# Optimization experiments

Measured on AMD Instinct MI355X. Metric: run time of the kernel, lower is better.

## Reference

```python
import jax, jax.numpy as jnp
import numpy as np

B, T, D = 4, 4096, 384
H = W = 64
K = 8            # num_clusters
CH = MH = 64     # conv_hidden, mlp_hidden
NL = 4           # num_layers
IN_DIM = D + 2   # use_spatial_pos
RADIUS_FRACTION = 30.0
GRAPH_EPS = 1e-6
SM_LAMBDA = 0.01
FS_LAMBDA = 0.09


def conv2d(x, w, b, groups=1):
    out = jax.lax.conv_general_dilated(x, w, (1, 1), 'SAME',
        dimension_numbers=('NCHW', 'OIHW', 'NCHW'), feature_group_count=groups)
    return out + b[None, :, None, None]


def group_norm(x, g, b, groups, eps=1e-5):
    n, c, h, w = x.shape
    xg = x.reshape(n, groups, c // groups, h, w)
    m = xg.mean(axis=(2, 3, 4), keepdims=True)
    v = xg.var(axis=(2, 3, 4), keepdims=True)
    xn = ((xg - m) * jax.lax.rsqrt(v + eps)).reshape(n, c, h, w)
    return xn * g[None, :, None, None] + b[None, :, None, None]


def layer_norm(x, g, b, eps=1e-5):
    m = x.mean(-1, keepdims=True)
    v = x.var(-1, keepdims=True)
    return (x - m) * jax.lax.rsqrt(v + eps) * g + b


def build_graph():
    # unit-square grid positions; radius graph with self loops; sym normalization
    lin = jnp.linspace(0.0, 1.0, H)
    gy, gx = jnp.meshgrid(lin, lin, indexing='ij')
    pos = jnp.stack([gx.reshape(-1), gy.reshape(-1)], axis=1)  # (T,2)
    r2 = 2.0 / (RADIUS_FRACTION * RADIUS_FRACTION)             # (sqrt(2)/rf)^2
    dx = pos[:, 0][:, None] - pos[:, 0][None, :]
    dy = pos[:, 1][:, None] - pos[:, 1][None, :]
    adj = ((dx * dx + dy * dy) <= r2).astype(jnp.float32)      # includes loop
    deg = adj.sum(1)
    dis = jnp.where(deg > 0, deg ** -0.5, 0.0)
    a_tilde = dis[:, None] * adj * dis[None, :]                # D^-1/2 A D^-1/2
    return pos, a_tilde


def setup_inputs():
    key = jax.random.key(0)
    ks = jax.random.split(key, 16)
    rn = lambda i, s, sc=0.05: jax.random.normal(ks[i], s, dtype=jnp.float32) * sc
    z = lambda s: jnp.zeros(s, jnp.float32)
    o = lambda s: jnp.ones(s, jnp.float32)
    return {
        'token_features': jax.random.normal(ks[0], (B, T, D), dtype=jnp.float32),
        'gcn_w0': rn(1, (IN_DIM, CH)), 'gcn_b0': z((CH,)),
        'gcn_w': rn(2, (NL - 1, CH, CH)), 'gcn_b': z((NL - 1, CH)),
        'ln_g': o((NL, CH)), 'ln_b': z((NL, CH)),
        'res_w': rn(3, (IN_DIM, CH)), 'res_b': z((CH,)),
        'res_ln_g': o((CH,)), 'res_ln_b': z((CH,)),
        'mlp_w1': rn(4, (CH, MH)), 'mlp_b1': z((MH,)),
        'mlp_ln_g': o((MH,)), 'mlp_ln_b': z((MH,)),
        'mlp_w2': rn(5, (MH, K)), 'mlp_b2': z((K,)),
        'sm_w1': rn(6, (K, 1, 3, 3)), 'sm_b1': z((K,)),
        'sm_gn1_g': o((K,)), 'sm_gn1_b': z((K,)),
        'sm_w2': rn(7, (K, 1, 3, 3)), 'sm_b2': z((K,)),
        'sm_gn2_g': o((K,)), 'sm_gn2_b': z((K,)),
        'ec_w1': rn(8, (32, D, 3, 3), 0.02), 'ec_b1': z((32,)),
        'ec_gn_g': o((32,)), 'ec_gn_b': z((32,)),
        'ec_w2': rn(9, (1, 32, 1, 1)), 'ec_b2': z((1,)),
        'k': 8,
    }


def reference(token_features, gcn_w0, gcn_b0, gcn_w, gcn_b, ln_g, ln_b,
              res_w, res_b, res_ln_g, res_ln_b, mlp_w1, mlp_b1, mlp_ln_g,
              mlp_ln_b, mlp_w2, mlp_b2, sm_w1, sm_b1, sm_gn1_g, sm_gn1_b,
              sm_w2, sm_b2, sm_gn2_g, sm_gn2_b, ec_w1, ec_b1, ec_gn_g,
              ec_gn_b, ec_w2, ec_b2, k):
    pos, A = build_graph()

    # ---- feature smoothness loss (edge-aware) ----
    fs = token_features.reshape(B, H, W, D).transpose(0, 3, 1, 2)  # (B,D,H,W)
    e = jax.nn.relu(group_norm(conv2d(fs, ec_w1, ec_b1), ec_gn_g, ec_gn_b, 8))
    ew = jax.nn.sigmoid(conv2d(e, ec_w2, ec_b2))                   # (B,1,H,W)
    gy = fs[:, :, 1:, :] - fs[:, :, :-1, :]
    gx = fs[:, :, :, 1:] - fs[:, :, :, :-1]
    loss_y = (gy * gy * ew[:, :, 1:, :]).mean() / D
    loss_x = (gx * gx * ew[:, :, :, 1:]).mean() / D
    feat_sm = (loss_y + loss_x) / 2

    # ---- GNN pool (batched; adjacency shared across batch) ----
    x = jnp.concatenate(
        [token_features, jnp.broadcast_to(pos[None], (B, T, 2))], axis=-1)
    Ws = [gcn_w0] + [gcn_w[i] for i in range(NL - 1)]
    bs = [gcn_b0] + [gcn_b[i] for i in range(NL - 1)]
    for i in range(NL):
        x_prev = x
        h = jnp.einsum('ts,bsc->btc', A, x @ Ws[i]) + bs[i]  # GCNConv
        h = jax.nn.elu(layer_norm(h, ln_g[i], ln_b[i]))
        if i == 0:
            x_prev = layer_norm(x_prev @ res_w + res_b, res_ln_g, res_ln_b)
        x = h + x_prev
    h1 = jax.nn.elu(layer_norm(x @ mlp_w1 + mlp_b1, mlp_ln_g, mlp_ln_b))
    S = jax.nn.softmax(h1 @ mlp_w2 + mlp_b2, axis=-1)        # (B,T,K)

    # ---- spatial smoothness loss (depthwise convs) ----
    S_sp = S.transpose(0, 2, 1).reshape(B, K, H, W)
    t = jax.nn.relu(group_norm(conv2d(S_sp, sm_w1, sm_b1, groups=K),
                               sm_gn1_g, sm_gn1_b, K))
    S_sm = group_norm(conv2d(t, sm_w2, sm_b2, groups=K), sm_gn2_g, sm_gn2_b, K)
    sm_loss = ((S_sm - S_sp) ** 2).mean(axis=(1, 2, 3))      # (B,)

    # ---- normalized-cut + orthogonality losses ----
    AS = jnp.einsum('ts,bsk->btk', A, S)
    num = jnp.einsum('btk,btk->b', S, AS)
    degA = A.sum(1)
    den = jnp.einsum('btk,t,btk->b', S, degA, S) + GRAPH_EPS
    loss_c = -num / den
    SS = jnp.einsum('btk,btl->bkl', S, S)
    ssn = jnp.sqrt((SS * SS).sum(axis=(1, 2)))
    eyeK = jnp.eye(K, dtype=jnp.float32)
    target = eyeK / (jnp.sqrt(jnp.float32(K)) + GRAPH_EPS)
    diff = SS / (ssn[:, None, None] + GRAPH_EPS) - target[None]
    loss_o = jnp.sqrt((diff * diff).sum(axis=(1, 2)))

    loss = (loss_c + loss_o + SM_LAMBDA * sm_loss).mean() + FS_LAMBDA * feat_sm
    return S, loss
```

## Files before the change

### kernel.cpp

```cpp
#include <hip/hip_runtime.h>
#include <hip/hip_bf16.h>


#define B_ 4
#define T_ 4096
#define D_ 384

typedef __attribute__((ext_vector_type(8))) short short8b;
typedef __attribute__((ext_vector_type(4))) float f32x4;

__device__ __forceinline__ float wred(float v) {
#pragma unroll
  for (int off = 32; off > 0; off >>= 1) v += __shfl_xor(v, off);
  return v;
}

__device__ __forceinline__ void wred2(float& a, float& b) {
#pragma unroll
  for (int off = 32; off > 0; off >>= 1) {
    a += __shfl_xor(a, off);
    b += __shfl_xor(b, off);
  }
}

__device__ __forceinline__ short bf16rne(float f) {
  unsigned u = __float_as_uint(f);
  unsigned r = (u + 0x7FFFu + ((u >> 16) & 1u)) >> 16;
  return (short)r;
}

__device__ __forceinline__ float bf2f(short s) {
  return __uint_as_float(((unsigned)(unsigned short)s) << 16);
}

__device__ __forceinline__ float uval(int i) {
  int c = (i < 2 ? i : 2) + ((63 - i) < 2 ? (63 - i) : 2) + 1;
  return rsqrtf((float)c);
}

struct PGcn {
  const float *feat, *ecw1, *w0, *resw, *resb, *resg, *reslb;
  const float *gw, *gb0, *gb, *lng, *lnb;
  const float *w1, *b1, *mlng, *mlnb, *w2, *b2;
  short *fb, *wq, *wb;
  float *accg, *xwA, *xwB, *xbuf, *resbuf, *S, *Sp;
};

struct PLoss {
  const float *S, *Sp;
  const float *smw1, *smb1, *smg1, *smbb1, *smw2, *smb2, *smg2, *smbb2;
  const short *fb, *wq;
  const float *ecb1;
  float *eraw, *accg;
  const float *gng, *gnb, *ecw2, *ecb2;
  float *ew, *outp;
};


__device__ __forceinline__ void prep_stage(int blk, int tid,
    const float* feat, const float* ecw1, const float* w0, const float* resw,
    short* fb, short* wq, short* wb, float* accg) {
  if (blk == 0) {
    accg[tid] = 0.f;
    accg[tid + 256] = 0.f;
  }
  if (blk < 3072) {
    int t = blk * 256 + tid;
    const float4* s = (const float4*)feat + (size_t)t * 2;
    float4 a = s[0], b = s[1];
    short8b v;
    v[0] = bf16rne(a.x); v[1] = bf16rne(a.y); v[2] = bf16rne(a.z); v[3] = bf16rne(a.w);
    v[4] = bf16rne(b.x); v[5] = bf16rne(b.y); v[6] = bf16rne(b.z); v[7] = bf16rne(b.w);
    *(short8b*)(fb + (size_t)t * 8) = v;
  } else if (blk < 3504) {
    int idx = (blk - 3072) * 256 + tid;
    int q = idx % 9;
    int rest = idx / 9;
    int d = rest % 384;
    int o = rest / 384;
    wq[((size_t)(q * 32 + o)) * 384 + d] = bf16rne(ecw1[idx]);
  } else {
    int u = (blk - 3504) * 256 + tid;
    int l = u & 63, f = (u >> 6) & 7, s = u >> 9;
    int c = f * 16 + (l & 15);
    int k0 = s * 32 + ((l >> 4) << 3);
    const float* src = (c < 64) ? (w0 + c) : (resw + (c - 64));
    short8b v;
#pragma unroll
    for (int j = 0; j < 8; ++j) v[j] = bf16rne(src[(size_t)(k0 + j) * 64]);
    *(short8b*)(wb + (size_t)u * 8) = v;
  }
}

__device__ __forceinline__ void gemm0_stage(char* smem, int blk, int tid,
    const short* fb, const short* wb, const float* w0, const float* resw,
    const float* resb, const float* resg, const float* reslb,
    float* xw, float* res) {
  short8b* Ab8 = (short8b*)smem;
  short8b* Bb8 = (short8b*)(smem + 24576);
  int row0 = blk * 32;
#pragma unroll
  for (int it = 0; it < 6; ++it) {
    int u = it * 256 + tid;
    int l = u & 63, s = (u >> 6) % 12, set = u / 768;
    int row = row0 + set * 16 + (l & 15);
    int k = s * 32 + ((l >> 4) << 3);
    Ab8[(set * 12 + s) * 64 + l] = *(const short8b*)(fb + (size_t)row * 384 + k);
  }
  int wid = tid >> 6, lane = tid & 63;
  int rowset = wid & 1, colhalf = wid >> 1;
  const short8b* wb8 = (const short8b*)wb;
  f32x4 acc[4];
#pragma unroll
  for (int f = 0; f < 4; ++f) acc[f] = (f32x4){0.f, 0.f, 0.f, 0.f};
  for (int c = 0; c < 3; ++c) {
    __syncthreads();
#pragma unroll
    for (int it = 0; it < 8; ++it) {
      int u = it * 256 + tid;
      Bb8[u] = wb8[c * 2048 + u];
    }
    __syncthreads();
#pragma unroll
    for (int s = 0; s < 4; ++s) {
      short8b av = Ab8[(rowset * 12 + c * 4 + s) * 64 + lane];
#pragma unroll
      for (int f = 0; f < 4; ++f) {
        short8b bv = Bb8[(s * 8 + colhalf * 4 + f) * 64 + lane];
        acc[f] = __builtin_amdgcn_mfma_f32_16x16x32_bf16(av, bv, acc[f], 0, 0, 0);
      }
    }
  }
  int g = lane >> 4, ln = lane & 15;
  if (colhalf == 0) {
    float pw1[4], pw2[4];
#pragma unroll
    for (int f = 0; f < 4; ++f) {
      int c = f * 16 + ln;
      pw1[f] = w0[384 * 64 + c];
      pw2[f] = w0[385 * 64 + c];
    }
#pragma unroll
    for (int r = 0; r < 4; ++r) {
      int grow = row0 + rowset * 16 + g * 4 + r;
      int t = grow & (T_ - 1);
      float px = (float)(t & 63) * (1.f / 63.f);
      float py = (float)(t >> 6) * (1.f / 63.f);
#pragma unroll
      for (int f = 0; f < 4; ++f)
        xw[(size_t)grow * 64 + f * 16 + ln] = acc[f][r] + px * pw1[f] + py * pw2[f];
    }
  } else {
    float rw1[4], rw2[4], rb[4], rgam[4], rbet[4];
#pragma unroll
    for (int f = 0; f < 4; ++f) {
      int c = f * 16 + ln;
      rw1[f] = resw[384 * 64 + c];
      rw2[f] = resw[385 * 64 + c];
      rb[f] = resb[c]; rgam[f] = resg[c]; rbet[f] = reslb[c];
    }
#pragma unroll
    for (int r = 0; r < 4; ++r) {
      int grow = row0 + rowset * 16 + g * 4 + r;
      int t = grow & (T_ - 1);
      float px = (float)(t & 63) * (1.f / 63.f);
      float py = (float)(t >> 6) * (1.f / 63.f);
      float rv[4];
      float s1 = 0.f, s2 = 0.f;
#pragma unroll
      for (int f = 0; f < 4; ++f) {
        float v = acc[f][r] + px * rw1[f] + py * rw2[f] + rb[f];
        rv[f] = v;
        s1 += v;
        s2 = fmaf(v, v, s2);
      }
#pragma unroll
      for (int off = 1; off < 16; off <<= 1) {
        s1 += __shfl_xor(s1, off);
        s2 += __shfl_xor(s2, off);
      }
      float mean = s1 * (1.f / 64.f);
      float var = s2 * (1.f / 64.f) - mean * mean;
      float inv = rsqrtf(var + 1e-5f);
#pragma unroll
      for (int f = 0; f < 4; ++f)
        res[(size_t)grow * 64 + f * 16 + ln] =
            (rv[f] - mean) * inv * rgam[f] + rbet[f];
    }
  }
}

__device__ __forceinline__ void layer_stage(char* smem, int blk, int tid,
    const float* xw_in, const float* W, const float* bias, const float* lng,
    const float* lnb, const float* resid, float* xout, float* xw_out) {
  float* sx = (float*)smem;
  float* sW = (float*)(smem + 8192);
  int t0 = blk * 32;
  int b = t0 >> 12, i = (t0 >> 6) & 63;
  const float4* w4 = (const float4*)W;
  float4* sW4 = (float4*)sW;
#pragma unroll
  for (int l = 0; l < 4; ++l) sW4[tid + l * 256] = w4[tid + l * 256];
  int c = tid & 63, jg = tid >> 6;
  int jb = (t0 & 63) + jg * 8;
  float ui = uval(i);
  float acc[8];
#pragma unroll
  for (int m = 0; m < 8; ++m) acc[m] = 0.f;
  float uw[12];
#pragma unroll
  for (int d = 0; d < 12; ++d) {
    int jj = jb - 2 + d;
    uw[d] = (jj >= 0 && jj < 64) ? uval(jj) : 0.f;
  }
#pragma unroll
  for (int di = -2; di <= 2; ++di) {
    int ii = i + di;
    if (ii < 0 || ii > 63) continue;
    float wi = uval(ii);
    const float* src = xw_in + ((size_t)((b << 12) + (ii << 6))) * 64 + c;
    float v[12];
#pragma unroll
    for (int d = 0; d < 12; ++d) {
      int jj = jb - 2 + d;
      v[d] = (jj >= 0 && jj < 64) ? src[jj * 64] : 0.f;
    }
#pragma unroll
    for (int m = 0; m < 8; ++m) {
      float t = v[m] * uw[m] + v[m + 1] * uw[m + 1] + v[m + 2] * uw[m + 2] +
                v[m + 3] * uw[m + 3] + v[m + 4] * uw[m + 4];
      acc[m] = fmaf(wi, t, acc[m]);
    }
  }
  float bc = bias[c], gam = lng[c], bet = lnb[c];
#pragma unroll
  for (int m = 0; m < 8; ++m) {
    int lrow = jg * 8 + m;
    float h = ui * uval(jb + m) * acc[m] + bc;
    float s1 = h, s2 = h * h;
    wred2(s1, s2);
    float mean = s1 * (1.f / 64.f);
    float var = s2 * (1.f / 64.f) - mean * mean;
    float n = (h - mean) * rsqrtf(var + 1e-5f) * gam + bet;
    float e = n > 0.f ? n : (expf(n) - 1.f);
    float xv = e + resid[(size_t)(t0 + lrow) * 64 + c];
    xout[(size_t)(t0 + lrow) * 64 + c] = xv;
    sx[lrow * 64 + c] = xv;
  }
  __syncthreads();
  float a[8];
#pragma unroll
  for (int m = 0; m < 8; ++m) a[m] = 0.f;
#pragma unroll
  for (int kq = 0; kq < 16; ++kq) {
    float4 fv[8];
#pragma unroll
    for (int m = 0; m < 8; ++m)
      fv[m] = *(const float4*)&sx[(jg * 8 + m) * 64 + kq * 4];
#pragma unroll
    for (int dk = 0; dk < 4; ++dk) {
      float wv = sW[(kq * 4 + dk) * 64 + c];
#pragma unroll
      for (int m = 0; m < 8; ++m)
        a[m] = fmaf(((const float*)&fv[m])[dk], wv, a[m]);
    }
  }
#pragma unroll
  for (int m = 0; m < 8; ++m)
    xw_out[(size_t)(t0 + jg * 8 + m) * 64 + c] = a[m];
}

__device__ __forceinline__ void st4mlp_stage(char* smem, int blk, int tid,
    const float* xw_in, const float* bias, const float* lng, const float* lnb,
    const float* resid, const float* w1, const float* b1, const float* mlng,
    const float* mlnb, const float* w2, const float* b2, float* S, float* Sp) {
  float* sx = (float*)smem;
  float* sW = (float*)(smem + 8192);
  float* sh = (float*)(smem + 24576);
  int t0 = blk * 32;
  int b = t0 >> 12, i = (t0 >> 6) & 63;
  const float4* w4 = (const float4*)w1;
  float4* sW4 = (float4*)sW;
#pragma unroll
  for (int l = 0; l < 4; ++l) sW4[tid + l * 256] = w4[tid + l * 256];
  int c = tid & 63, jg = tid >> 6;
  int jb = (t0 & 63) + jg * 8;
  float ui = uval(i);
  float acc[8];
#pragma unroll
  for (int m = 0; m < 8; ++m) acc[m] = 0.f;
  float uw[12];
#pragma unroll
  for (int d = 0; d < 12; ++d) {
    int jj = jb - 2 + d;
    uw[d] = (jj >= 0 && jj < 64) ? uval(jj) : 0.f;
  }
#pragma unroll
  for (int di = -2; di <= 2; ++di) {
    int ii = i + di;
    if (ii < 0 || ii > 63) continue;
    float wi = uval(ii);
    const float* src = xw_in + ((size_t)((b << 12) + (ii << 6))) * 64 + c;
    float v[12];
#pragma unroll
    for (int d = 0; d < 12; ++d) {
      int jj = jb - 2 + d;
      v[d] = (jj >= 0 && jj < 64) ? src[jj * 64] : 0.f;
    }
#pragma unroll
    for (int m = 0; m < 8; ++m) {
      float t = v[m] * uw[m] + v[m + 1] * uw[m + 1] + v[m + 2] * uw[m + 2] +
                v[m + 3] * uw[m + 3] + v[m + 4] * uw[m + 4];
      acc[m] = fmaf(wi, t, acc[m]);
    }
  }
  float bc = bias[c], gam = lng[c], bet = lnb[c];
#pragma unroll
  for (int m = 0; m < 8; ++m) {
    int lrow = jg * 8 + m;
    float h = ui * uval(jb + m) * acc[m] + bc;
    float s1 = h, s2 = h * h;
    wred2(s1, s2);
    float mean = s1 * (1.f / 64.f);
    float var = s2 * (1.f / 64.f) - mean * mean;
    float n = (h - mean) * rsqrtf(var + 1e-5f) * gam + bet;
    float e = n > 0.f ? n : (expf(n) - 1.f);
    sx[lrow * 64 + c] = e + resid[(size_t)(t0 + lrow) * 64 + c];
  }
  __syncthreads();
  float a[8];
#pragma unroll
  for (int m = 0; m < 8; ++m) a[m] = 0.f;
#pragma unroll
  for (int kq = 0; kq < 16; ++kq) {
    float4 fv[8];
#pragma unroll
    for (int m = 0; m < 8; ++m)
      fv[m] = *(const float4*)&sx[(jg * 8 + m) * 64 + kq * 4];
#pragma unroll
    for (int dk = 0; dk < 4; ++dk) {
      float wv = sW[(kq * 4 + dk) * 64 + c];
#pragma unroll
      for (int m = 0; m < 8; ++m)
        a[m] = fmaf(((const float*)&fv[m])[dk], wv, a[m]);
    }
  }
  float mb = b1[c], mgam = mlng[c], mbet = mlnb[c];
#pragma unroll
  for (int m = 0; m < 8; ++m) {
    float h = a[m] + mb;
    float s1 = h, s2 = h * h;
    wred2(s1, s2);
    float mean = s1 * (1.f / 64.f);
    float var = s2 * (1.f / 64.f) - mean * mean;
    float n = (h - mean) * rsqrtf(var + 1e-5f) * mgam + mbet;
    sh[(jg * 8 + m) * 64 + c] = n > 0.f ? n : (expf(n) - 1.f);
  }
  __syncthreads();
  int k = tid & 7, j = tid >> 3;
  float lg = b2[k];
#pragma unroll 8
  for (int u = 0; u < 64; ++u) {
    int cc = (u + j * 8) & 63;
    lg = fmaf(sh[j * 64 + cc], w2[cc * 8 + k], lg);
  }
  float mx = lg;
  mx = fmaxf(mx, __shfl_xor(mx, 1));
  mx = fmaxf(mx, __shfl_xor(mx, 2));
  mx = fmaxf(mx, __shfl_xor(mx, 4));
  float ex = expf(lg - mx);
  float sum = ex;
  sum += __shfl_xor(sum, 1);
  sum += __shfl_xor(sum, 2);
  sum += __shfl_xor(sum, 4);
  float val = ex / sum;
  int grow = t0 + j;
  int t = grow & (T_ - 1);
  S[(size_t)grow * 8 + k] = val;
  Sp[((size_t)((b << 3) + k) << 12) + t] = val;
}

__device__ __forceinline__ void cut_stage(char* smem, int blk, int tid,
    const float* S, float* accg) {
  {
    int k = tid & 7;
    int tl = tid >> 3;
    int gid = blk * 32 + tl;
    int b = gid >> 12, t = gid & (T_ - 1);
    int i = t >> 6, j = t & 63;
    float ui = uval(i), uj = uval(j);
    float as = 0.f, sui = 0.f, suj = 0.f;
#pragma unroll
    for (int di = -2; di <= 2; ++di) {
      int ii = i + di;
      if (ii < 0 || ii > 63) continue;
      float wi = uval(ii);
      sui += wi;
#pragma unroll
      for (int dj = -2; dj <= 2; ++dj) {
        int jj = j + dj;
        if (jj < 0 || jj > 63) continue;
        as = fmaf(wi * uval(jj),
                  S[((size_t)((b << 12) + (ii << 6) + jj)) * 8 + k], as);
      }
    }
#pragma unroll
    for (int dj = -2; dj <= 2; ++dj) {
      int jj = j + dj;
      if (jj >= 0 && jj <= 63) suj += uval(jj);
    }
    as *= ui * uj;
    float sv = S[(size_t)gid * 8 + k];
    float degA = ui * uj * sui * suj;
    float numv = sv * as, denv = sv * sv * degA;
    wred2(numv, denv);
    float* lds = (float*)smem;
    int wid = tid >> 6, lane = tid & 63;
    if (lane == 0) { lds[wid * 2] = numv; lds[wid * 2 + 1] = denv; }
    __syncthreads();
    if (tid == 0) {
      int slot = b * 4 + (blk & 3);
      atomicAdd(&accg[slot], lds[0] + lds[2] + lds[4] + lds[6]);
      atomicAdd(&accg[16 + slot], lds[1] + lds[3] + lds[5] + lds[7]);
    }
  }
  if (blk < 32) {
    __syncthreads();
    int b = blk >> 3, chunk = blk & 7;
    int wid = tid >> 6, lane = tid & 63;
    int kk = lane >> 3, ll = lane & 7;
    int t0 = chunk * 512 + wid * 128;
    float a = 0.f;
    const float* Sb = S + ((size_t)b << 12) * 8;
    for (int it = 0; it < 128; ++it) {
      const float* sr = Sb + (size_t)(t0 + it) * 8;
      a = fmaf(sr[kk], sr[ll], a);
    }
    float* lds2 = (float*)smem;
    lds2[tid] = a;
    __syncthreads();
    if (tid < 64) {
      float s = lds2[tid] + lds2[tid + 64] + lds2[tid + 128] + lds2[tid + 192];
      atomicAdd(&accg[128 + b * 64 + tid], s);
    }
  }
}

__device__ __forceinline__ void sm_stage(char* smem, int bk, int tid,
    const float* Sp, const float* w1, const float* b1, const float* g1,
    const float* bb1, const float* w2, const float* b2, const float* g2,
    const float* bb2, float* accg) {
  float* p0 = (float*)smem;
  float* p1 = p0 + 4096;
  float* red = p1 + 4096;
  int b = bk >> 3, k = bk & 7;
  const float4* src = (const float4*)(Sp + (size_t)bk * 4096);
  float4* d0 = (float4*)p0;
  for (int i2 = tid; i2 < 1024; i2 += 256) d0[i2] = src[i2];
  float W1[9], W2[9];
#pragma unroll
  for (int q = 0; q < 9; ++q) { W1[q] = w1[k * 9 + q]; W2[q] = w2[k * 9 + q]; }
  __syncthreads();
  int wid = tid >> 6, lane = tid & 63;
  float y[16];
  float s1 = 0.f, s2 = 0.f;
#pragma unroll
  for (int v = 0; v < 16; ++v) {
    int p = v * 256 + tid;
    int i2 = p >> 6, j2 = p & 63;
    float a = b1[k];
#pragma unroll
    for (int dy = 0; dy < 3; ++dy) {
      int ii = i2 + dy - 1;
      if (ii < 0 || ii > 63) continue;
#pragma unroll
      for (int dx = 0; dx < 3; ++dx) {
        int jj = j2 + dx - 1;
        if (jj < 0 || jj > 63) continue;
        a = fmaf(W1[dy * 3 + dx], p0[(ii << 6) + jj], a);
      }
    }
    y[v] = a;
    s1 += a;
    s2 = fmaf(a, a, s2);
  }
  wred2(s1, s2);
  if (lane == 0) { red[wid * 2] = s1; red[wid * 2 + 1] = s2; }
  __syncthreads();
  float mean = (red[0] + red[2] + red[4] + red[6]) * (1.f / 4096.f);
  float var = (red[1] + red[3] + red[5] + red[7]) * (1.f / 4096.f) - mean * mean;
  float inv = rsqrtf(var + 1e-5f) * g1[k];
  float sh = bb1[k];
  __syncthreads();
#pragma unroll
  for (int v = 0; v < 16; ++v) {
    int p = v * 256 + tid;
    p1[p] = fmaxf((y[v] - mean) * inv + sh, 0.f);
  }
  __syncthreads();
  s1 = 0.f; s2 = 0.f;
#pragma unroll
  for (int v = 0; v < 16; ++v) {
    int p = v * 256 + tid;
    int i2 = p >> 6, j2 = p & 63;
    float a = b2[k];
#pragma unroll
    for (int dy = 0; dy < 3; ++dy) {
      int ii = i2 + dy - 1;
      if (ii < 0 || ii > 63) continue;
#pragma unroll
      for (int dx = 0; dx < 3; ++dx) {
        int jj = j2 + dx - 1;
        if (jj < 0 || jj > 63) continue;
        a = fmaf(W2[dy * 3 + dx], p1[(ii << 6) + jj], a);
      }
    }
    y[v] = a;
    s1 += a;
    s2 = fmaf(a, a, s2);
  }
  wred2(s1, s2);
  if (lane == 0) { red[wid * 2] = s1; red[wid * 2 + 1] = s2; }
  __syncthreads();
  float mean2 = (red[0] + red[2] + red[4] + red[6]) * (1.f / 4096.f);
  float var2 = (red[1] + red[3] + red[5] + red[7]) * (1.f / 4096.f) - mean2 * mean2;
  float inv2 = rsqrtf(var2 + 1e-5f) * g2[k];
  float sh2 = bb2[k];
  float sd = 0.f;
#pragma unroll
  for (int v = 0; v < 16; ++v) {
    int p = v * 256 + tid;
    float sm = (y[v] - mean2) * inv2 + sh2;
    float dd = sm - p0[p];
    sd = fmaf(dd, dd, sd);
  }
  sd = wred(sd);
  __syncthreads();
  if (lane == 0) red[wid] = sd;
  __syncthreads();
  if (tid == 0)
    atomicAdd(&accg[384 + b * 2 + (bk & 1)],
              (red[0] + red[1] + red[2] + red[3]) * (1.f / 32768.f));
}

__device__ __forceinline__ void ecconv_stage(char* smem, int blk2, int tid,
    const short* fb, const short* wq, const float* ecb1, float* eraw,
    float* accg) {
  short* Abuf = (short*)smem;
  short* Wbuf = Abuf + 6432;
  float* sW1 = (float*)(Wbuf + 9216);
  float* sW2 = sW1 + 128;
  int b = blk2 >> 6, i = blk2 & 63;
  int wid = tid >> 6, lane = tid & 63;
  int m = lane & 15, kg = lane >> 4;
  if (tid < 36) {
    int zkg = tid & 3, sl = (tid >> 2) % 3, r = tid / 12;
    int slot = sl == 0 ? 0 : (sl == 1 ? 65 : 66);
    *(short8b*)&Abuf[(r * 67 + slot) * 32 + zkg * 8] = (short8b)0;
  }
  f32x4 acc0 = {0.f, 0.f, 0.f, 0.f};
  f32x4 acc1 = {0.f, 0.f, 0.f, 0.f};
  int abase = (wid * 16 + m) * 32 + kg * 8;
  int bbase = m * 32 + kg * 8;
  for (int c = 0; c < 12; ++c) {
    __syncthreads();
#pragma unroll
    for (int s = 0; s < 3; ++s) {
      int cid = tid + (s << 8);
      int akg = cid & 3, px = (cid >> 2) & 63, r = cid >> 8;
      int ii = i + r - 1;
      short8b v = (short8b)0;
      if (ii >= 0 && ii < 64)
        v = *(const short8b*)(fb +
              ((size_t)((b << 12) + (ii << 6) + px)) * D_ + c * 32 + akg * 8);
      *(short8b*)&Abuf[(r * 67 + px + 1) * 32 + akg * 8] = v;
    }
    for (int l = tid; l < 1152; l += 256) {
      int wkg = l & 3, oo = (l >> 2) & 31, q = l >> 7;
      short8b wv =
          *(const short8b*)(wq + ((size_t)(q * 32 + oo)) * D_ + c * 32 + wkg * 8);
      *(short8b*)&Wbuf[(q * 32 + oo) * 32 + wkg * 8] = wv;
    }
    __syncthreads();
#pragma unroll
    for (int q = 0; q < 9; ++q) {
      short8b av = *(const short8b*)&Abuf[abase + ((q / 3) * 67 + (q % 3)) * 32];
      short8b bv0 = *(const short8b*)&Wbuf[bbase + q * 1024];
      short8b bv1 = *(const short8b*)&Wbuf[bbase + q * 1024 + 512];
      acc0 = __builtin_amdgcn_mfma_f32_16x16x32_bf16(av, bv0, acc0, 0, 0, 0);
      acc1 = __builtin_amdgcn_mfma_f32_16x16x32_bf16(av, bv1, acc1, 0, 0, 0);
    }
  }
  int o0 = m, o1 = 16 + m;
  float bs0 = ecb1[o0], bs1 = ecb1[o1];
  float s1a = 0.f, s2a = 0.f, s1b = 0.f, s2b = 0.f;
  int jbase = wid * 16 + kg * 4;
#pragma unroll
  for (int rg = 0; rg < 4; ++rg) {
    float v0 = acc0[rg] + bs0;
    float v1 = acc1[rg] + bs1;
    int j = jbase + rg;
    size_t px = ((size_t)((b << 12) + (i << 6) + j)) * 32;
    eraw[px + o0] = v0;
    eraw[px + o1] = v1;
    s1a += v0; s2a = fmaf(v0, v0, s2a);
    s1b += v1; s2b = fmaf(v1, v1, s2b);
  }
  s1a += __shfl_xor(s1a, 16); s1a += __shfl_xor(s1a, 32);
  s2a += __shfl_xor(s2a, 16); s2a += __shfl_xor(s2a, 32);
  s1b += __shfl_xor(s1b, 16); s1b += __shfl_xor(s1b, 32);
  s2b += __shfl_xor(s2b, 16); s2b += __shfl_xor(s2b, 32);
  if (lane < 16) {
    sW1[wid * 32 + lane] = s1a; sW2[wid * 32 + lane] = s2a;
    sW1[wid * 32 + lane + 16] = s1b; sW2[wid * 32 + lane + 16] = s2b;
  }
  __syncthreads();
  if (tid < 32) {
    float t1 = sW1[tid] + sW1[32 + tid] + sW1[64 + tid] + sW1[96 + tid];
    float t2 = sW2[tid] + sW2[32 + tid] + sW2[64 + tid] + sW2[96 + tid];
    t1 += __shfl_xor(t1, 1); t1 += __shfl_xor(t1, 2);
    t2 += __shfl_xor(t2, 1); t2 += __shfl_xor(t2, 2);
    if ((tid & 3) == 0) {
      atomicAdd(&accg[64 + b * 16 + (tid >> 2) * 2], t1);
      atomicAdd(&accg[64 + b * 16 + (tid >> 2) * 2 + 1], t2);
    }
  }
}

__device__ __forceinline__ void ecfinal_stage(char* smem, int blk, int tid,
    const float* eraw, const float* accg, const float* gng, const float* gnb,
    const float* w2, const float* b2, float* ew) {
  float* st = (float*)smem;
  int idx = blk * 256 + tid;
  int b = idx >> 12;
  if (tid < 16) st[tid] = accg[64 + b * 16 + tid];
  __syncthreads();
  float a = b2[0];
  const float4* er = (const float4*)(eraw + (size_t)idx * 32);
#pragma unroll
  for (int oq = 0; oq < 8; ++oq) {
    float mean = st[oq * 2] * (1.f / 16384.f);
    float var = st[oq * 2 + 1] * (1.f / 16384.f) - mean * mean;
    float inv = rsqrtf(var + 1e-5f);
    float4 e = er[oq];
    int o = oq * 4;
    float v0 = (e.x - mean) * inv * gng[o + 0] + gnb[o + 0];
    float v1 = (e.y - mean) * inv * gng[o + 1] + gnb[o + 1];
    float v2 = (e.z - mean) * inv * gng[o + 2] + gnb[o + 2];
    float v3 = (e.w - mean) * inv * gng[o + 3] + gnb[o + 3];
    a = fmaf(fmaxf(v0, 0.f), w2[o + 0], a);
    a = fmaf(fmaxf(v1, 0.f), w2[o + 1], a);
    a = fmaf(fmaxf(v2, 0.f), w2[o + 2], a);
    a = fmaf(fmaxf(v3, 0.f), w2[o + 3], a);
  }
  ew[idx] = 1.f / (1.f + expf(-a));
}

__device__ __forceinline__ void fsloss_stage(char* smem, int blk, int tid,
    const short* fb, const float* ew, float* accg) {
  float sy = 0.f, sx = 0.f;
  const int N = B_ * T_ * 48;
  for (int idx = blk * 256 + tid; idx < N; idx += 512 * 256) {
    int d8 = idx % 48;
    int rt = idx / 48;
    int t = rt & (T_ - 1);
    int i = t >> 6, j = t & 63;
    const short8b* fp = (const short8b*)(fb + (size_t)rt * D_) + d8;
    short8b f0 = *fp;
    if (i < 63) {
      short8b f1 = fp[64 * 48];
      float w = ew[rt + 64];
      float a = 0.f;
#pragma unroll
      for (int u = 0; u < 8; ++u) {
        float d = bf2f(f1[u]) - bf2f(f0[u]);
        a = fmaf(d, d, a);
      }
      sy += w * a;
    }
    if (j < 63) {
      short8b f1 = fp[48];
      float w = ew[rt + 1];
      float a = 0.f;
#pragma unroll
      for (int u = 0; u < 8; ++u) {
        float d = bf2f(f1[u]) - bf2f(f0[u]);
        a = fmaf(d, d, a);
      }
      sx += w * a;
    }
  }
  wred2(sy, sx);
  float* lds = (float*)smem;
  int wid = tid >> 6, lane = tid & 63;
  if (lane == 0) { lds[wid * 2] = sy; lds[wid * 2 + 1] = sx; }
  __syncthreads();
  if (tid == 0) {
    int slot = 32 + (blk & 15) * 2;
    atomicAdd(&accg[slot], lds[0] + lds[2] + lds[4] + lds[6]);
    atomicAdd(&accg[slot + 1], lds[1] + lds[3] + lds[5] + lds[7]);
  }
}

__device__ __forceinline__ void final_stage(const float* accg, float* out) {
  float total = 0.f;
  for (int b = 0; b < 4; ++b) {
    const float* SSb = accg + 128 + b * 64;
    float ssq = 0.f;
    for (int v = 0; v < 64; ++v) ssq += SSb[v] * SSb[v];
    float ssn = sqrtf(ssq);
    float tgt = 1.f / (sqrtf(8.f) + 1e-6f);
    float inv = 1.f / (ssn + 1e-6f);
    float lo = 0.f;
    for (int kk = 0; kk < 8; ++kk)
      for (int ll = 0; ll < 8; ++ll) {
        float dd = SSb[kk * 8 + ll] * inv - (kk == ll ? tgt : 0.f);
        lo += dd * dd;
      }
    lo = sqrtf(lo);
    float num = accg[b * 4] + accg[b * 4 + 1] + accg[b * 4 + 2] + accg[b * 4 + 3];
    float den = accg[16 + b * 4] + accg[16 + b * 4 + 1] + accg[16 + b * 4 + 2] +
                accg[16 + b * 4 + 3];
    float lc = -num / (den + 1e-6f);
    float smv = accg[384 + b * 2] + accg[385 + b * 2];
    total += lc + lo + 0.01f * smv;
  }
  total *= 0.25f;
  float fsy = 0.f, fsx = 0.f;
  for (int s = 0; s < 16; ++s) { fsy += accg[32 + s * 2]; fsx += accg[33 + s * 2]; }
  const float cnt = 4.f * 384.f * 63.f * 64.f;
  float ly = fsy / cnt * (1.f / 384.f);
  float lx = fsx / cnt * (1.f / 384.f);
  out[131072] = total + 0.09f * 0.5f * (ly + lx);
}


__global__ __launch_bounds__(256) void k_prep_sa(PGcn p) {
  prep_stage(blockIdx.x, threadIdx.x, p.feat, p.ecw1, p.w0, p.resw, p.fb, p.wq,
             p.wb, p.accg);
}
__global__ __launch_bounds__(256) void k_gemm0_sa(PGcn p) {
  __shared__ __align__(16) char smem[57344];
  gemm0_stage(smem, blockIdx.x, threadIdx.x, p.fb, p.wb, p.w0, p.resw, p.resb,
              p.resg, p.reslb, p.xwA, p.resbuf);
}
__global__ __launch_bounds__(256) void k_layer_sa(PGcn p, int l) {
  __shared__ __align__(16) char smem[24576];
  const float* xin = (l == 1) ? p.xwB : p.xwA;
  float* xwout = (l == 1) ? p.xwA : p.xwB;
  const float* resid = (l == 0) ? p.resbuf : p.xbuf;
  const float* W = p.gw + l * 4096;
  const float* bias = (l == 0) ? p.gb0 : (p.gb + (l - 1) * 64);
  layer_stage(smem, blockIdx.x, threadIdx.x, xin, W, bias, p.lng + l * 64,
              p.lnb + l * 64, resid, p.xbuf, xwout);
}
__global__ __launch_bounds__(256) void k_st4mlp_sa(PGcn p) {
  __shared__ __align__(16) char smem[32768];
  st4mlp_stage(smem, blockIdx.x, threadIdx.x, p.xwB, p.gb + 128, p.lng + 192,
               p.lnb + 192, p.xbuf, p.w1, p.b1, p.mlng, p.mlnb, p.w2, p.b2,
               p.S, p.Sp);
}
__global__ __launch_bounds__(256) void k_lossmix_sa(PLoss p) {
  __shared__ __align__(16) char smem[32832];
  int blk = blockIdx.x, tid = threadIdx.x;
  if (blk < 512)
    cut_stage(smem, blk, tid, p.S, p.accg);
  else if (blk < 544)
    sm_stage(smem, blk - 512, tid, p.Sp, p.smw1, p.smb1, p.smg1, p.smbb1,
             p.smw2, p.smb2, p.smg2, p.smbb2, p.accg);
  else
    ecconv_stage(smem, blk - 544, tid, p.fb, p.wq, p.ecb1, p.eraw, p.accg);
}
__global__ __launch_bounds__(256) void k_ecfinal_sa(PLoss p) {
  __shared__ __align__(16) char smem[64];
  ecfinal_stage(smem, blockIdx.x, threadIdx.x, p.eraw, p.accg, p.gng, p.gnb,
                p.ecw2, p.ecb2, p.ew);
}
__global__ __launch_bounds__(256) void k_fsloss_sa(PLoss p) {
  __shared__ __align__(16) char smem[32];
  fsloss_stage(smem, blockIdx.x, threadIdx.x, p.fb, p.ew, p.accg);
}
__global__ void k_final_sa(PLoss p) {
  if (threadIdx.x == 0 && blockIdx.x == 0) final_stage(p.accg, p.outp);
}


extern "C" void kernel_launch(void* const* d_in, const int* in_sizes, int n_in,
                              void* d_out, int out_size, void* d_ws, size_t ws_size,
                              hipStream_t stream) {
  const float* feat = (const float*)d_in[0];
  const float* gcn_w0 = (const float*)d_in[1];
  const float* gcn_b0 = (const float*)d_in[2];
  const float* gcn_w = (const float*)d_in[3];
  const float* gcn_b = (const float*)d_in[4];
  const float* ln_g = (const float*)d_in[5];
  const float* ln_b = (const float*)d_in[6];
  const float* res_w = (const float*)d_in[7];
  const float* res_b = (const float*)d_in[8];
  const float* res_ln_g = (const float*)d_in[9];
  const float* res_ln_b = (const float*)d_in[10];
  const float* mlp_w1 = (const float*)d_in[11];
  const float* mlp_b1 = (const float*)d_in[12];
  const float* mlp_ln_g = (const float*)d_in[13];
  const float* mlp_ln_b = (const float*)d_in[14];
  const float* mlp_w2 = (const float*)d_in[15];
  const float* mlp_b2 = (const float*)d_in[16];
  const float* sm_w1 = (const float*)d_in[17];
  const float* sm_b1 = (const float*)d_in[18];
  const float* sm_g1 = (const float*)d_in[19];
  const float* sm_bb1 = (const float*)d_in[20];
  const float* sm_w2 = (const float*)d_in[21];
  const float* sm_b2 = (const float*)d_in[22];
  const float* sm_g2 = (const float*)d_in[23];
  const float* sm_bb2 = (const float*)d_in[24];
  const float* ec_w1 = (const float*)d_in[25];
  const float* ec_b1 = (const float*)d_in[26];
  const float* ec_gn_g = (const float*)d_in[27];
  const float* ec_gn_b = (const float*)d_in[28];
  const float* ec_w2 = (const float*)d_in[29];
  const float* ec_b2 = (const float*)d_in[30];

  float* out = (float*)d_out;
  float* ws = (float*)d_ws;
  float* acc = ws;
  float* xwA = ws + 512;
  float* xwB = xwA + 1048576;
  float* xbuf = xwB + 1048576;
  float* resbuf = xbuf + 1048576;
  float* Sp = resbuf + 1048576;
  float* eraw = Sp + 131072;
  float* ew = eraw + 524288;
  short* wqb = (short*)(ew + 16384);
  short* wb = wqb + 110592;
  short* fb = wb + 49152;
  float* S = out;

  PGcn pg = {feat, ec_w1, gcn_w0, res_w, res_b, res_ln_g, res_ln_b,
             gcn_w, gcn_b0, gcn_b, ln_g, ln_b,
             mlp_w1, mlp_b1, mlp_ln_g, mlp_ln_b, mlp_w2, mlp_b2,
             fb, wqb, wb, acc, xwA, xwB, xbuf, resbuf, S, Sp};
  PLoss pl = {S, Sp, sm_w1, sm_b1, sm_g1, sm_bb1, sm_w2, sm_b2, sm_g2, sm_bb2,
              fb, wqb, ec_b1, eraw, acc, ec_gn_g, ec_gn_b, ec_w2, ec_b2, ew,
              out};

  k_prep_sa<<<3528, 256, 0, stream>>>(pg);
  k_gemm0_sa<<<512, 256, 0, stream>>>(pg);
  k_layer_sa<<<512, 256, 0, stream>>>(pg, 0);
  k_layer_sa<<<512, 256, 0, stream>>>(pg, 1);
  k_layer_sa<<<512, 256, 0, stream>>>(pg, 2);
  k_st4mlp_sa<<<512, 256, 0, stream>>>(pg);
  k_lossmix_sa<<<800, 256, 0, stream>>>(pl);
  k_ecfinal_sa<<<64, 256, 0, stream>>>(pl);
  k_fsloss_sa<<<512, 256, 0, stream>>>(pl);
  k_final_sa<<<1, 64, 0, stream>>>(pl);
}
```

Before: 139.3 us.

## Co-schedule edge-conv loss stages with GCN layers and halve layer tile size

Moves the independent edge-conv, ecfinal and feature-smoothness loss stages out of the tail and merges them into the same launches as gemm0 and the first two GCN layers. Independent work from both chains can then share the GPU and the launch count drops from ten to eight. The layer stage now handles 16 rows per block instead of 32, which doubles its grid and shrinks shared memory to raise occupancy. The cost is more redundant halo loads and weight staging per block, and every stage must keep the correct dependencies across the new grouping.

```diff
diff --git a/kernel.cpp b/kernel.cpp
--- a/kernel.cpp
+++ b/kernel.cpp
@@ -194,22 +194,22 @@
     const float* xw_in, const float* W, const float* bias, const float* lng,
     const float* lnb, const float* resid, float* xout, float* xw_out) {
   float* sx = (float*)smem;
-  float* sW = (float*)(smem + 8192);
-  int t0 = blk * 32;
+  float* sW = (float*)(smem + 4096);
+  int t0 = blk * 16;
   int b = t0 >> 12, i = (t0 >> 6) & 63;
   const float4* w4 = (const float4*)W;
   float4* sW4 = (float4*)sW;
 #pragma unroll
   for (int l = 0; l < 4; ++l) sW4[tid + l * 256] = w4[tid + l * 256];
   int c = tid & 63, jg = tid >> 6;
-  int jb = (t0 & 63) + jg * 8;
+  int jb = (t0 & 63) + jg * 4;
   float ui = uval(i);
-  float acc[8];
-#pragma unroll
-  for (int m = 0; m < 8; ++m) acc[m] = 0.f;
-  float uw[12];
-#pragma unroll
-  for (int d = 0; d < 12; ++d) {
+  float acc[4];
+#pragma unroll
+  for (int m = 0; m < 4; ++m) acc[m] = 0.f;
+  float uw[8];
+#pragma unroll
+  for (int d = 0; d < 8; ++d) {
     int jj = jb - 2 + d;
     uw[d] = (jj >= 0 && jj < 64) ? uval(jj) : 0.f;
   }
@@ -219,14 +219,14 @@
     if (ii < 0 || ii > 63) continue;
     float wi = uval(ii);
     const float* src = xw_in + ((size_t)((b << 12) + (ii << 6))) * 64 + c;
-    float v[12];
-#pragma unroll
-    for (int d = 0; d < 12; ++d) {
+    float v[8];
+#pragma unroll
+    for (int d = 0; d < 8; ++d) {
       int jj = jb - 2 + d;
       v[d] = (jj >= 0 && jj < 64) ? src[jj * 64] : 0.f;
     }
 #pragma unroll
-    for (int m = 0; m < 8; ++m) {
+    for (int m = 0; m < 4; ++m) {
       float t = v[m] * uw[m] + v[m + 1] * uw[m + 1] + v[m + 2] * uw[m + 2] +
                 v[m + 3] * uw[m + 3] + v[m + 4] * uw[m + 4];
       acc[m] = fmaf(wi, t, acc[m]);
@@ -234,8 +234,8 @@
   }
   float bc = bias[c], gam = lng[c], bet = lnb[c];
 #pragma unroll
-  for (int m = 0; m < 8; ++m) {
-    int lrow = jg * 8 + m;
+  for (int m = 0; m < 4; ++m) {
+    int lrow = jg * 4 + m;
     float h = ui * uval(jb + m) * acc[m] + bc;
     float s1 = h, s2 = h * h;
     wred2(s1, s2);
@@ -248,26 +248,26 @@
     sx[lrow * 64 + c] = xv;
   }
   __syncthreads();
-  float a[8];
-#pragma unroll
-  for (int m = 0; m < 8; ++m) a[m] = 0.f;
+  float a[4];
+#pragma unroll
+  for (int m = 0; m < 4; ++m) a[m] = 0.f;
 #pragma unroll
   for (int kq = 0; kq < 16; ++kq) {
-    float4 fv[8];
-#pragma unroll
-    for (int m = 0; m < 8; ++m)
-      fv[m] = *(const float4*)&sx[(jg * 8 + m) * 64 + kq * 4];
+    float4 fv[4];
+#pragma unroll
+    for (int m = 0; m < 4; ++m)
+      fv[m] = *(const float4*)&sx[(jg * 4 + m) * 64 + kq * 4];
 #pragma unroll
     for (int dk = 0; dk < 4; ++dk) {
       float wv = sW[(kq * 4 + dk) * 64 + c];
 #pragma unroll
-      for (int m = 0; m < 8; ++m)
+      for (int m = 0; m < 4; ++m)
         a[m] = fmaf(((const float*)&fv[m])[dk], wv, a[m]);
     }
   }
 #pragma unroll
-  for (int m = 0; m < 8; ++m)
-    xw_out[(size_t)(t0 + jg * 8 + m) * 64 + c] = a[m];
+  for (int m = 0; m < 4; ++m)
+    xw_out[(size_t)(t0 + jg * 4 + m) * 64 + c] = a[m];
 }
 
 __device__ __forceinline__ void st4mlp_stage(char* smem, int blk, int tid,
@@ -735,52 +735,63 @@
 }
 
 
-__global__ __launch_bounds__(256) void k_prep_sa(PGcn p) {
+__global__ __launch_bounds__(256) void k_prep(PGcn p) {
   prep_stage(blockIdx.x, threadIdx.x, p.feat, p.ecw1, p.w0, p.resw, p.fb, p.wq,
              p.wb, p.accg);
 }
-__global__ __launch_bounds__(256) void k_gemm0_sa(PGcn p) {
+
+__global__ __launch_bounds__(256) void k_mix1(PGcn g, PLoss l) {
   __shared__ __align__(16) char smem[57344];
-  gemm0_stage(smem, blockIdx.x, threadIdx.x, p.fb, p.wb, p.w0, p.resw, p.resb,
-              p.resg, p.reslb, p.xwA, p.resbuf);
-}
-__global__ __launch_bounds__(256) void k_layer_sa(PGcn p, int l) {
-  __shared__ __align__(16) char smem[24576];
-  const float* xin = (l == 1) ? p.xwB : p.xwA;
-  float* xwout = (l == 1) ? p.xwA : p.xwB;
-  const float* resid = (l == 0) ? p.resbuf : p.xbuf;
-  const float* W = p.gw + l * 4096;
-  const float* bias = (l == 0) ? p.gb0 : (p.gb + (l - 1) * 64);
-  layer_stage(smem, blockIdx.x, threadIdx.x, xin, W, bias, p.lng + l * 64,
-              p.lnb + l * 64, resid, p.xbuf, xwout);
-}
-__global__ __launch_bounds__(256) void k_st4mlp_sa(PGcn p) {
+  if (blockIdx.x < 256)
+    ecconv_stage(smem, blockIdx.x, threadIdx.x, l.fb, l.wq, l.ecb1, l.eraw,
+                 l.accg);
+  else
+    gemm0_stage(smem, blockIdx.x - 256, threadIdx.x, g.fb, g.wb, g.w0, g.resw,
+                g.resb, g.resg, g.reslb, g.xwA, g.resbuf);
+}
+
+__global__ __launch_bounds__(256) void k_mix2(PGcn g, PLoss l) {
+  __shared__ __align__(16) char smem[20480];
+  if (blockIdx.x < 64)
+    ecfinal_stage(smem, blockIdx.x, threadIdx.x, l.eraw, l.accg, l.gng, l.gnb,
+                  l.ecw2, l.ecb2, l.ew);
+  else
+    layer_stage(smem, blockIdx.x - 64, threadIdx.x, g.xwA, g.gw, g.gb0, g.lng,
+                g.lnb, g.resbuf, g.xbuf, g.xwB);
+}
+
+__global__ __launch_bounds__(256) void k_mix3(PGcn g, PLoss l) {
+  __shared__ __align__(16) char smem[20480];
+  if (blockIdx.x < 512)
+    fsloss_stage(smem, blockIdx.x, threadIdx.x, l.fb, l.ew, l.accg);
+  else
+    layer_stage(smem, blockIdx.x - 512, threadIdx.x, g.xwB, g.gw + 4096, g.gb,
+                g.lng + 64, g.lnb + 64, g.xbuf, g.xbuf, g.xwA);
+}
+
+__global__ __launch_bounds__(256) void k_layer2(PGcn p) {
+  __shared__ __align__(16) char smem[20480];
+  layer_stage(smem, blockIdx.x, threadIdx.x, p.xwA, p.gw + 8192, p.gb + 64,
+              p.lng + 128, p.lnb + 128, p.xbuf, p.xbuf, p.xwB);
+}
+
+__global__ __launch_bounds__(256) void k_st4mlp(PGcn p) {
   __shared__ __align__(16) char smem[32768];
   st4mlp_stage(smem, blockIdx.x, threadIdx.x, p.xwB, p.gb + 128, p.lng + 192,
                p.lnb + 192, p.xbuf, p.w1, p.b1, p.mlng, p.mlnb, p.w2, p.b2,
                p.S, p.Sp);
 }
-__global__ __launch_bounds__(256) void k_lossmix_sa(PLoss p) {
+
+__global__ __launch_bounds__(256) void k_cutsm(PLoss p) {
   __shared__ __align__(16) char smem[32832];
-  int blk = blockIdx.x, tid = threadIdx.x;
-  if (blk < 512)
-    cut_stage(smem, blk, tid, p.S, p.accg);
-  else if (blk < 544)
-    sm_stage(smem, blk - 512, tid, p.Sp, p.smw1, p.smb1, p.smg1, p.smbb1,
-             p.smw2, p.smb2, p.smg2, p.smbb2, p.accg);
+  if (blockIdx.x < 512)
+    cut_stage(smem, blockIdx.x, threadIdx.x, p.S, p.accg);
   else
-    ecconv_stage(smem, blk - 544, tid, p.fb, p.wq, p.ecb1, p.eraw, p.accg);
-}
-__global__ __launch_bounds__(256) void k_ecfinal_sa(PLoss p) {
-  __shared__ __align__(16) char smem[64];
-  ecfinal_stage(smem, blockIdx.x, threadIdx.x, p.eraw, p.accg, p.gng, p.gnb,
-                p.ecw2, p.ecb2, p.ew);
-}
-__global__ __launch_bounds__(256) void k_fsloss_sa(PLoss p) {
-  __shared__ __align__(16) char smem[32];
-  fsloss_stage(smem, blockIdx.x, threadIdx.x, p.fb, p.ew, p.accg);
-}
-__global__ void k_final_sa(PLoss p) {
+    sm_stage(smem, blockIdx.x - 512, threadIdx.x, p.Sp, p.smw1, p.smb1, p.smg1,
+             p.smbb1, p.smw2, p.smb2, p.smg2, p.smbb2, p.accg);
+}
+
+__global__ void k_final(PLoss p) {
   if (threadIdx.x == 0 && blockIdx.x == 0) final_stage(p.accg, p.outp);
 }
 
@@ -843,14 +854,12 @@
               fb, wqb, ec_b1, eraw, acc, ec_gn_g, ec_gn_b, ec_w2, ec_b2, ew,
               out};
 
-  k_prep_sa<<<3528, 256, 0, stream>>>(pg);
-  k_gemm0_sa<<<512, 256, 0, stream>>>(pg);
-  k_layer_sa<<<512, 256, 0, stream>>>(pg, 0);
-  k_layer_sa<<<512, 256, 0, stream>>>(pg, 1);
-  k_layer_sa<<<512, 256, 0, stream>>>(pg, 2);
-  k_st4mlp_sa<<<512, 256, 0, stream>>>(pg);
-  k_lossmix_sa<<<800, 256, 0, stream>>>(pl);
-  k_ecfinal_sa<<<64, 256, 0, stream>>>(pl);
-  k_fsloss_sa<<<512, 256, 0, stream>>>(pl);
-  k_final_sa<<<1, 64, 0, stream>>>(pl);
-}
+  k_prep<<<3528, 256, 0, stream>>>(pg);
+  k_mix1<<<768, 256, 0, stream>>>(pg, pl);
+  k_mix2<<<1088, 256, 0, stream>>>(pg, pl);
+  k_mix3<<<1536, 256, 0, stream>>>(pg, pl);
+  k_layer2<<<1024, 256, 0, stream>>>(pg);
+  k_st4mlp<<<512, 256, 0, stream>>>(pg);
+  k_cutsm<<<544, 256, 0, stream>>>(pl);
+  k_final<<<1, 64, 0, stream>>>(pl);
+}
```

New measurement: 124.7 us, median of 2. 10.5% less time.
